# Performance work log

Hardware: AMD Instinct MI355X
Metric: run time of the kernel (lower is better)

Reference implementation:

```python
import jax, jax.numpy as jnp
import numpy as np

N = 50000   # nodes
E = 800000  # edges (avg degree 16)
C = 96      # in = hidden = out channels


def setup_inputs() -> dict:
    key = jax.random.key(0)
    ks = jax.random.split(key, 8)
    s = np.float32(1.0 / np.sqrt(C))
    x = jax.random.normal(ks[0], (N, C), dtype=jnp.float32)
    edge_index = jax.random.randint(ks[1], (2, E), 0, N, dtype=jnp.int64)
    W1 = jax.random.normal(ks[2], (C, C), dtype=jnp.float32) * s
    Wr1 = jax.random.normal(ks[3], (C, C), dtype=jnp.float32) * s
    b1 = jnp.zeros((C,), dtype=jnp.float32)
    W2 = jax.random.normal(ks[4], (C, C), dtype=jnp.float32) * s
    Wr2 = jax.random.normal(ks[5], (C, C), dtype=jnp.float32) * s
    b2 = jnp.zeros((C,), dtype=jnp.float32)
    return {"x": x, "edge_index": edge_index,
            "W1": W1, "Wr1": Wr1, "b1": b1,
            "W2": W2, "Wr2": Wr2, "b2": b2}


def spline_conv(x, edge_index, W, W_root, b):
    """Gather-transform-scatter message passing (SplineConv core, mean aggr)."""
    src, dst = edge_index[0], edge_index[1]
    h = x @ W                                   # [N, C] transform once per node
    msg = h[src]                                # [E, C] edge gather
    agg = jax.ops.segment_sum(msg, dst, num_segments=N)        # scatter-add
    deg = jax.ops.segment_sum(jnp.ones((E,), x.dtype), dst, num_segments=N)
    agg = agg / jnp.maximum(deg, 1.0)[:, None]  # mean aggregation
    return agg + x @ W_root + b                 # root weight + bias


def reference(x, edge_index, W1, Wr1, b1, W2, Wr2, b2):
    h = jax.nn.relu(spline_conv(x, edge_index, W1, Wr1, b1))
    out = spline_conv(h, edge_index, W2, Wr2, b2)
    return out.reshape(-1)  # generalization of x.view(1600)
```

## Files before the change

### kernel.cpp

```cpp
#include <hip/hip_runtime.h>

#define C 96
#define BKT_SHIFT 9
#define BKT_SIZE 512
#define CAP 10240
#define EB 2048
typedef unsigned char u8;
typedef unsigned short u16;
typedef unsigned int u32;
typedef __attribute__((ext_vector_type(8))) short short8;
typedef __attribute__((ext_vector_type(4))) float floatx4;
typedef __attribute__((ext_vector_type(2))) float floatx2;

__device__ inline u16 f2bf(float f) {
    union { float f; u32 u; } v; v.f = f;
    u32 r = v.u + 0x7fff + ((v.u >> 16) & 1);
    return (u16)(r >> 16);
}
__device__ inline u32 pk4_fp8(float a, float b, float c, float d) {
    u32 w = 0;
    w = __builtin_amdgcn_cvt_pk_fp8_f32(a, b, w, false);
    w = __builtin_amdgcn_cvt_pk_fp8_f32(c, d, w, true);
    return w;
}
__device__ inline u8 f2fp8(float a) {
    return (u8)(__builtin_amdgcn_cvt_pk_fp8_f32(a, a, 0, false) & 0xff);
}

__global__ __launch_bounds__(128) void zero_kernel(int* __restrict__ bkt_cnt) {
    bkt_cnt[threadIdx.x] = 0;
}

__global__ __launch_bounds__(256) void binA_kernel(const int* __restrict__ src,
                                                   const int* __restrict__ dst,
                                                   int* __restrict__ bkt_cnt,
                                                   u32* __restrict__ stage, int E, int DB,
                                                   const float* __restrict__ x,
                                                   u16* __restrict__ xb,
                                                   u8* __restrict__ xf8, int n16, int CX,
                                                   const float* W0, const float* W1,
                                                   const float* W2, const float* W3,
                                                   u16* T0, u16* T1, u16* T2, u16* T3) {
    int bid = blockIdx.x;
    int t = threadIdx.x;
    if (bid >= DB) {
        if (bid < DB + CX) {
            int i = (bid - DB) * 256 + t;
            if (i >= n16) return;
            const float4* p = (const float4*)x + (size_t)i * 4;
            float4 a = p[0], b = p[1], c = p[2], d = p[3];
            short8 o0, o1;
            o0[0] = (short)f2bf(a.x); o0[1] = (short)f2bf(a.y);
            o0[2] = (short)f2bf(a.z); o0[3] = (short)f2bf(a.w);
            o0[4] = (short)f2bf(b.x); o0[5] = (short)f2bf(b.y);
            o0[6] = (short)f2bf(b.z); o0[7] = (short)f2bf(b.w);
            o1[0] = (short)f2bf(c.x); o1[1] = (short)f2bf(c.y);
            o1[2] = (short)f2bf(c.z); o1[3] = (short)f2bf(c.w);
            o1[4] = (short)f2bf(d.x); o1[5] = (short)f2bf(d.y);
            o1[6] = (short)f2bf(d.z); o1[7] = (short)f2bf(d.w);
            *(short8*)(xb + (size_t)i * 16) = o0;
            *(short8*)(xb + (size_t)i * 16 + 8) = o1;
            uint4 f8;
            f8.x = pk4_fp8(a.x, a.y, a.z, a.w);
            f8.y = pk4_fp8(b.x, b.y, b.z, b.w);
            f8.z = pk4_fp8(c.x, c.y, c.z, c.w);
            f8.w = pk4_fp8(d.x, d.y, d.z, d.w);
            *(uint4*)(xf8 + (size_t)i * 16) = f8;
        } else {
            int w = bid - DB - CX;
            const float* W = w == 0 ? W0 : w == 1 ? W1 : w == 2 ? W2 : W3;
            u16* T = w == 0 ? T0 : w == 1 ? T1 : w == 2 ? T2 : T3;
            for (int i = t; i < C * C; i += 256) {
                int k = i / C, n = i - k * C;
                T[n * C + k] = f2bf(W[i]);
            }
        }
        return;
    }

    __shared__ u32 s_word[EB];
    __shared__ u32 s_addr[EB];
    __shared__ int s_cnt[128];
    __shared__ int s_inc[128];
    __shared__ int s_base[128];
    int e0 = bid * EB;
    int cnt_here = min(EB, E - e0);

    for (int i = t; i < 128; i += 256) s_cnt[i] = 0;
    __syncthreads();

    int my_src[EB / 256], my_dl[EB / 256], my_b[EB / 256], my_rank[EB / 256];
    int nmine = 0;
#pragma unroll
    for (int k = 0; k < EB / 256; k++) {
        int i = t + k * 256;
        if (i < cnt_here) {
            int s = src[e0 + i], d = dst[e0 + i];
            int b = d >> BKT_SHIFT;
            my_src[nmine] = s;
            my_dl[nmine] = d & (BKT_SIZE - 1);
            my_b[nmine] = b;
            my_rank[nmine] = atomicAdd(&s_cnt[b], 1);
            nmine++;
        }
    }
    __syncthreads();

    if (t < 128) s_inc[t] = s_cnt[t];
    __syncthreads();
    for (int off = 1; off < 128; off <<= 1) {
        int x2 = (t >= off && t < 128) ? s_inc[t - off] : 0;
        __syncthreads();
        if (t < 128) s_inc[t] += x2;
        __syncthreads();
    }

    if (t < 128 && s_cnt[t] > 0)
        s_base[t] = t * CAP + atomicAdd(&bkt_cnt[t], s_cnt[t]);
    __syncthreads();

    for (int k = 0; k < nmine; k++) {
        int b = my_b[k];
        int slot = (s_inc[b] - s_cnt[b]) + my_rank[k];
        s_word[slot] = ((u32)my_dl[k] << 16) | (u32)my_src[k];
        s_addr[slot] = (u32)(s_base[b] + my_rank[k]);
    }
    __syncthreads();

    for (int i = t; i < cnt_here; i += 256) stage[s_addr[i]] = s_word[i];
}

__global__ __launch_bounds__(256) void binB_kernel(const u32* __restrict__ stage,
                                                   const int* __restrict__ bkt_cnt,
                                                   int* __restrict__ deg,
                                                   int* __restrict__ row_off,
                                                   u16* __restrict__ csr, int N) {
    __shared__ int cnt[BKT_SIZE];
    __shared__ int cur[BKT_SIZE];
    __shared__ int ssum[256];
    int b = blockIdx.x;
    int n0 = b << BKT_SHIFT;
    int nn = min(BKT_SIZE, N - n0);
    int t = threadIdx.x;
    int s0 = b * CAP;
    int s1 = s0 + bkt_cnt[b];

    for (int i = t; i < BKT_SIZE; i += 256) cnt[i] = 0;
    __syncthreads();

    for (int i = s0 + t; i < s1; i += 256) atomicAdd(&cnt[stage[i] >> 16], 1);
    __syncthreads();

    int a0 = cnt[2 * t], a1 = cnt[2 * t + 1];
    ssum[t] = a0 + a1;
    __syncthreads();
    for (int off = 1; off < 256; off <<= 1) {
        int x = (t >= off) ? ssum[t - off] : 0;
        __syncthreads();
        ssum[t] += x;
        __syncthreads();
    }
    int excl = ssum[t] - (a0 + a1);
    cur[2 * t] = s0 + excl;
    cur[2 * t + 1] = s0 + excl + a0;
    if (2 * t < nn) { deg[n0 + 2 * t] = a0; row_off[n0 + 2 * t] = s0 + excl; }
    if (2 * t + 1 < nn) { deg[n0 + 2 * t + 1] = a1; row_off[n0 + 2 * t + 1] = s0 + excl + a0; }
    __syncthreads();

    for (int i = s0 + t; i < s1; i += 256) {
        u32 w = stage[i];
        int p = atomicAdd(&cur[w >> 16], 1);
        csr[p] = (u16)(w & 0xffffu);
    }
}

template <bool RELU, bool WF8, typename OT>
__global__ __launch_bounds__(256, 4) void layer_kernel(const u16* __restrict__ Xbf,
                                                       const u8* __restrict__ Xf8,
                                                       const int* __restrict__ row_off,
                                                       const int* __restrict__ deg,
                                                       const u16* __restrict__ csr,
                                                       const u16* __restrict__ WTA,
                                                       const u16* __restrict__ WTR,
                                                       const float* __restrict__ BIAS,
                                                       OT* __restrict__ Y,
                                                       u8* __restrict__ Yf8, int n) {
    __shared__ u16 sA[64 * 104];
    __shared__ int s_dg[64];
    __shared__ int s_perm[64];
    const int t = threadIdx.x;
    const int row0 = blockIdx.x * 64;

    if (t < 64) {
        int node = row0 + t;
        s_dg[t] = (node < n) ? deg[node] : 0;
    }
    __syncthreads();
    if (t < 64) {
        int di = s_dg[t];
        int r = 0;
#pragma unroll 8
        for (int j = 0; j < 64; j++) {
            int dj = s_dg[j];
            r += (dj < di) || (dj == di && j < t);
        }
        s_perm[r] = t;
    }
    __syncthreads();

    {
        int nl = s_perm[t >> 2];
        int node = row0 + nl;
        int q = t & 3;
        float acc[24];
#pragma unroll
        for (int i = 0; i < 24; i++) acc[i] = 0.f;
        int d = 0;
        if (node < n) {
            int start = row_off[node];
            d = s_dg[nl];
            const u8* Xq = Xf8 + q * 24;
            int j = 0;
            for (; j + 4 <= d; j += 4) {
                int si[4];
#pragma unroll
                for (int k = 0; k < 4; k++) si[k] = csr[start + j + k];
                uint2 v[4][3];
#pragma unroll
                for (int k = 0; k < 4; k++) {
                    const u8* p = Xq + (size_t)si[k] * 96;
                    v[k][0] = *(const uint2*)(p);
                    v[k][1] = *(const uint2*)(p + 8);
                    v[k][2] = *(const uint2*)(p + 16);
                }
#pragma unroll
                for (int k = 0; k < 4; k++) {
                    u32 ws[6] = {v[k][0].x, v[k][0].y, v[k][1].x,
                                 v[k][1].y, v[k][2].x, v[k][2].y};
#pragma unroll
                    for (int i = 0; i < 6; i++) {
                        floatx2 lo = __builtin_amdgcn_cvt_pk_f32_fp8(ws[i], false);
                        floatx2 hi = __builtin_amdgcn_cvt_pk_f32_fp8(ws[i], true);
                        acc[4 * i]     += lo[0];
                        acc[4 * i + 1] += lo[1];
                        acc[4 * i + 2] += hi[0];
                        acc[4 * i + 3] += hi[1];
                    }
                }
            }
            for (; j < d; j++) {
                const u8* p = Xq + (size_t)csr[start + j] * 96;
                u32 ws[6];
                uint2 w0 = *(const uint2*)(p);
                uint2 w1 = *(const uint2*)(p + 8);
                uint2 w2 = *(const uint2*)(p + 16);
                ws[0] = w0.x; ws[1] = w0.y; ws[2] = w1.x;
                ws[3] = w1.y; ws[4] = w2.x; ws[5] = w2.y;
#pragma unroll
                for (int i = 0; i < 6; i++) {
                    floatx2 lo = __builtin_amdgcn_cvt_pk_f32_fp8(ws[i], false);
                    floatx2 hi = __builtin_amdgcn_cvt_pk_f32_fp8(ws[i], true);
                    acc[4 * i]     += lo[0];
                    acc[4 * i + 1] += lo[1];
                    acc[4 * i + 2] += hi[0];
                    acc[4 * i + 3] += hi[1];
                }
            }
        }
        float inv = 1.0f / fmaxf((float)d, 1.0f);
        u16* dl = sA + nl * 104 + q * 24;
#pragma unroll
        for (int c = 0; c < 3; c++) {
            short8 o;
#pragma unroll
            for (int i = 0; i < 8; i++) o[i] = (short)f2bf(acc[c * 8 + i] * inv);
            *(short8*)(dl + c * 8) = o;
        }
    }
    __syncthreads();

    const int lane = t & 63;
    const int w = t >> 6;
    const int quad = lane >> 4;
    const int l16 = lane & 15;
    const int r0 = row0 + w * 16;

    floatx4 acc6[6];
#pragma unroll
    for (int i = 0; i < 6; i++) acc6[i] = (floatx4){0.f, 0.f, 0.f, 0.f};

    {
        const u16* Ap = sA + (w * 16 + l16) * 104 + quad * 8;
        const u16* Wp = WTA + l16 * C + quad * 8;
#pragma unroll
        for (int ks = 0; ks < 3; ks++) {
            short8 a = *(const short8*)(Ap + ks * 32);
#pragma unroll
            for (int nt = 0; nt < 6; nt++) {
                short8 b = *(const short8*)(Wp + nt * 16 * C + ks * 32);
                acc6[nt] = __builtin_amdgcn_mfma_f32_16x16x32_bf16(a, b, acc6[nt], 0, 0, 0);
            }
        }
    }
    {
        int arow = r0 + l16;
        if (arow >= n) arow = n - 1;
        const u16* Xp = Xbf + (size_t)arow * C + quad * 8;
        const u16* Wp = WTR + l16 * C + quad * 8;
#pragma unroll
        for (int ks = 0; ks < 3; ks++) {
            short8 a = *(const short8*)(Xp + ks * 32);
#pragma unroll
            for (int nt = 0; nt < 6; nt++) {
                short8 b = *(const short8*)(Wp + nt * 16 * C + ks * 32);
                acc6[nt] = __builtin_amdgcn_mfma_f32_16x16x32_bf16(a, b, acc6[nt], 0, 0, 0);
            }
        }
    }

#pragma unroll
    for (int nt = 0; nt < 6; nt++) {
        int cc = nt * 16 + l16;
        float bv = BIAS[cc];
#pragma unroll
        for (int r = 0; r < 4; r++) {
            int row = r0 + quad * 4 + r;
            if (row >= n) continue;
            float v = acc6[nt][r] + bv;
            if (RELU) v = fmaxf(v, 0.f);
            if constexpr (sizeof(OT) == 2) Y[(size_t)row * C + cc] = (OT)f2bf(v);
            else                           Y[(size_t)row * C + cc] = (OT)v;
            if constexpr (WF8) Yf8[(size_t)row * 96 + cc] = f2fp8(v);
        }
    }
}

extern "C" void kernel_launch(void* const* d_in, const int* in_sizes, int n_in,
                              void* d_out, int out_size, void* d_ws, size_t ws_size,
                              hipStream_t stream) {
    const float* x   = (const float*)d_in[0];
    const int*   ei  = (const int*)d_in[1];
    const float* W1  = (const float*)d_in[2];
    const float* Wr1 = (const float*)d_in[3];
    const float* b1  = (const float*)d_in[4];
    const float* W2  = (const float*)d_in[5];
    const float* Wr2 = (const float*)d_in[6];
    const float* b2  = (const float*)d_in[7];
    float* out = (float*)d_out;

    const int N = in_sizes[0] / C;
    const int E = in_sizes[1] / 2;
    const int* src = ei;
    const int* dst = ei + E;

    const int nbkt = (N + BKT_SIZE - 1) >> BKT_SHIFT;
    int Npad = (N + 63) & ~63;

    int*   bkt_cnt = (int*)d_ws;
    int*   deg     = bkt_cnt + 128;
    int*   row_off = deg + Npad;
    u32*   stage   = (u32*)(row_off + Npad);
    u16*   csr     = (u16*)(stage + (size_t)nbkt * CAP);
    u16*   xb      = csr + (((size_t)nbkt * CAP + 7) & ~(size_t)7);
    u16*   h1b     = xb + (size_t)N * C;
    u16*   wt      = h1b + (size_t)N * C;
    u16 *wt1 = wt, *wtr1 = wt + C * C, *wt2 = wt + 2 * C * C, *wtr2 = wt + 3 * C * C;
    u8*    xf8     = (u8*)(wt + 4 * C * C);
    u8*    h1f8    = xf8 + (size_t)N * 96;

    const int grid64 = (N + 63) / 64;
    const int n16    = N * C / 16;
    const int CX     = (n16 + 255) / 256;
    const int DB     = (E + EB - 1) / EB;

    zero_kernel<<<1, 128, 0, stream>>>(bkt_cnt);
    binA_kernel<<<DB + CX + 4, 256, 0, stream>>>(src, dst, bkt_cnt, stage, E, DB,
                                                 x, xb, xf8, n16, CX,
                                                 W1, Wr1, W2, Wr2, wt1, wtr1, wt2, wtr2);
    binB_kernel<<<nbkt, 256, 0, stream>>>(stage, bkt_cnt, deg, row_off, csr, N);

    layer_kernel<true, true, u16><<<grid64, 256, 0, stream>>>(
        xb, xf8, row_off, deg, csr, wt1, wtr1, b1, h1b, h1f8, N);
    layer_kernel<false, false, float><<<grid64, 256, 0, stream>>>(
        h1b, h1f8, row_off, deg, csr, wt2, wtr2, b2, out, h1f8, N);
}
```

Measured before the change: 185.5 us.

## Replace global bucket atomics with per-block run tables read by CSR builder

The edge-binning pass no longer reserves slots with global atomics or scatters to per-bucket regions. Each block now writes its locally sorted edges contiguously and records per-bucket counts and offsets, so the zero kernel launch disappears. The CSR builder instead walks the 391 per-block runs for its bucket. In that loop each thread handles one short run serially, which may reduce parallelism and coalescing in the second pass.

```diff
diff --git a/kernel.cpp b/kernel.cpp
--- a/kernel.cpp
+++ b/kernel.cpp
@@ -27,13 +27,10 @@
     return (u8)(__builtin_amdgcn_cvt_pk_fp8_f32(a, a, 0, false) & 0xff);
 }
 
-__global__ __launch_bounds__(128) void zero_kernel(int* __restrict__ bkt_cnt) {
-    bkt_cnt[threadIdx.x] = 0;
-}
-
 __global__ __launch_bounds__(256) void binA_kernel(const int* __restrict__ src,
                                                    const int* __restrict__ dst,
-                                                   int* __restrict__ bkt_cnt,
+                                                   int* __restrict__ blk_cnt,
+                                                   int* __restrict__ blk_off,
                                                    u32* __restrict__ stage, int E, int DB,
                                                    const float* __restrict__ x,
                                                    u16* __restrict__ xb,
@@ -79,10 +76,8 @@
     }
 
     __shared__ u32 s_word[EB];
-    __shared__ u32 s_addr[EB];
     __shared__ int s_cnt[128];
     __shared__ int s_inc[128];
-    __shared__ int s_base[128];
     int e0 = bid * EB;
     int cnt_here = min(EB, E - e0);
 
@@ -114,27 +109,27 @@
         if (t < 128) s_inc[t] += x2;
         __syncthreads();
     }
-
-    if (t < 128 && s_cnt[t] > 0)
-        s_base[t] = t * CAP + atomicAdd(&bkt_cnt[t], s_cnt[t]);
-    __syncthreads();
+    if (t < 128) {
+        blk_cnt[bid * 128 + t] = s_cnt[t];
+        blk_off[bid * 128 + t] = s_inc[t] - s_cnt[t];
+    }
 
     for (int k = 0; k < nmine; k++) {
         int b = my_b[k];
         int slot = (s_inc[b] - s_cnt[b]) + my_rank[k];
         s_word[slot] = ((u32)my_dl[k] << 16) | (u32)my_src[k];
-        s_addr[slot] = (u32)(s_base[b] + my_rank[k]);
-    }
-    __syncthreads();
-
-    for (int i = t; i < cnt_here; i += 256) stage[s_addr[i]] = s_word[i];
+    }
+    __syncthreads();
+
+    for (int i = t; i < cnt_here; i += 256) stage[(size_t)bid * EB + i] = s_word[i];
 }
 
 __global__ __launch_bounds__(256) void binB_kernel(const u32* __restrict__ stage,
-                                                   const int* __restrict__ bkt_cnt,
+                                                   const int* __restrict__ blk_cnt,
+                                                   const int* __restrict__ blk_off,
                                                    int* __restrict__ deg,
                                                    int* __restrict__ row_off,
-                                                   u16* __restrict__ csr, int N) {
+                                                   u16* __restrict__ csr, int N, int DB) {
     __shared__ int cnt[BKT_SIZE];
     __shared__ int cur[BKT_SIZE];
     __shared__ int ssum[256];
@@ -143,12 +138,15 @@
     int nn = min(BKT_SIZE, N - n0);
     int t = threadIdx.x;
     int s0 = b * CAP;
-    int s1 = s0 + bkt_cnt[b];
 
     for (int i = t; i < BKT_SIZE; i += 256) cnt[i] = 0;
     __syncthreads();
 
-    for (int i = s0 + t; i < s1; i += 256) atomicAdd(&cnt[stage[i] >> 16], 1);
+    for (int i = t; i < DB; i += 256) {
+        int len = blk_cnt[i * 128 + b];
+        const u32* run = stage + (size_t)i * EB + blk_off[i * 128 + b];
+        for (int j = 0; j < len; j++) atomicAdd(&cnt[run[j] >> 16], 1);
+    }
     __syncthreads();
 
     int a0 = cnt[2 * t], a1 = cnt[2 * t + 1];
@@ -161,16 +159,21 @@
         __syncthreads();
     }
     int excl = ssum[t] - (a0 + a1);
+    if (2 * t < nn) { deg[n0 + 2 * t] = a0; row_off[n0 + 2 * t] = s0 + excl; }
+    if (2 * t + 1 < nn) { deg[n0 + 2 * t + 1] = a1; row_off[n0 + 2 * t + 1] = s0 + excl + a0; }
+    __syncthreads();
     cur[2 * t] = s0 + excl;
     cur[2 * t + 1] = s0 + excl + a0;
-    if (2 * t < nn) { deg[n0 + 2 * t] = a0; row_off[n0 + 2 * t] = s0 + excl; }
-    if (2 * t + 1 < nn) { deg[n0 + 2 * t + 1] = a1; row_off[n0 + 2 * t + 1] = s0 + excl + a0; }
-    __syncthreads();
-
-    for (int i = s0 + t; i < s1; i += 256) {
-        u32 w = stage[i];
-        int p = atomicAdd(&cur[w >> 16], 1);
-        csr[p] = (u16)(w & 0xffffu);
+    __syncthreads();
+
+    for (int i = t; i < DB; i += 256) {
+        int len = blk_cnt[i * 128 + b];
+        const u32* run = stage + (size_t)i * EB + blk_off[i * 128 + b];
+        for (int j = 0; j < len; j++) {
+            u32 w = run[j];
+            int p = atomicAdd(&cur[w >> 16], 1);
+            csr[p] = (u16)(w & 0xffffu);
+        }
     }
 }
 
@@ -250,12 +253,10 @@
             }
             for (; j < d; j++) {
                 const u8* p = Xq + (size_t)csr[start + j] * 96;
-                u32 ws[6];
                 uint2 w0 = *(const uint2*)(p);
                 uint2 w1 = *(const uint2*)(p + 8);
                 uint2 w2 = *(const uint2*)(p + 16);
-                ws[0] = w0.x; ws[1] = w0.y; ws[2] = w1.x;
-                ws[3] = w1.y; ws[4] = w2.x; ws[5] = w2.y;
+                u32 ws[6] = {w0.x, w0.y, w1.x, w1.y, w2.x, w2.y};
 #pragma unroll
                 for (int i = 0; i < 6; i++) {
                     floatx2 lo = __builtin_amdgcn_cvt_pk_f32_fp8(ws[i], false);
@@ -354,30 +355,30 @@
     const int* dst = ei + E;
 
     const int nbkt = (N + BKT_SIZE - 1) >> BKT_SHIFT;
+    const int DB   = (E + EB - 1) / EB;
+    const int n16  = N * C / 16;
+    const int CX   = (n16 + 255) / 256;
     int Npad = (N + 63) & ~63;
 
-    int*   bkt_cnt = (int*)d_ws;
-    int*   deg     = bkt_cnt + 128;
-    int*   row_off = deg + Npad;
-    u32*   stage   = (u32*)(row_off + Npad);
-    u16*   csr     = (u16*)(stage + (size_t)nbkt * CAP);
-    u16*   xb      = csr + (((size_t)nbkt * CAP + 7) & ~(size_t)7);
-    u16*   h1b     = xb + (size_t)N * C;
-    u16*   wt      = h1b + (size_t)N * C;
+    int*  blk_cnt = (int*)d_ws;
+    int*  blk_off = blk_cnt + DB * 128;
+    int*  deg     = blk_off + DB * 128;
+    int*  row_off = deg + Npad;
+    u32*  stage   = (u32*)(row_off + Npad);
+    u16*  csr     = (u16*)(stage + (size_t)DB * EB);
+    u16*  xb      = csr + (((size_t)nbkt * CAP + 7) & ~(size_t)7);
+    u16*  h1b     = xb + (size_t)N * C;
+    u16*  wt      = h1b + (size_t)N * C;
     u16 *wt1 = wt, *wtr1 = wt + C * C, *wt2 = wt + 2 * C * C, *wtr2 = wt + 3 * C * C;
-    u8*    xf8     = (u8*)(wt + 4 * C * C);
-    u8*    h1f8    = xf8 + (size_t)N * 96;
+    u8*   xf8     = (u8*)(wt + 4 * C * C);
+    u8*   h1f8    = xf8 + (size_t)N * 96;
 
     const int grid64 = (N + 63) / 64;
-    const int n16    = N * C / 16;
-    const int CX     = (n16 + 255) / 256;
-    const int DB     = (E + EB - 1) / EB;
-
-    zero_kernel<<<1, 128, 0, stream>>>(bkt_cnt);
-    binA_kernel<<<DB + CX + 4, 256, 0, stream>>>(src, dst, bkt_cnt, stage, E, DB,
+
+    binA_kernel<<<DB + CX + 4, 256, 0, stream>>>(src, dst, blk_cnt, blk_off, stage, E, DB,
                                                  x, xb, xf8, n16, CX,
                                                  W1, Wr1, W2, Wr2, wt1, wtr1, wt2, wtr2);
-    binB_kernel<<<nbkt, 256, 0, stream>>>(stage, bkt_cnt, deg, row_off, csr, N);
+    binB_kernel<<<nbkt, 256, 0, stream>>>(stage, blk_cnt, blk_off, deg, row_off, csr, N, DB);
 
     layer_kernel<true, true, u16><<<grid64, 256, 0, stream>>>(
         xb, xf8, row_off, deg, csr, wt1, wtr1, b1, h1b, h1f8, N);
```

After: 174.2 us. 6.1% less time.
